# Optimization experiments

Hardware: AMD Instinct MI355X
Metric: run time of the kernel (lower is better)

## Reference

```python
import jax, jax.numpy as jnp
import numpy as np

B, N, M, T, D, NH = 64, 1024, 32, 8, 512, 8
OUT = 1000
NSO, NSA = N // 4, N // 8
DH = D // NH


def _conv(x, w, b):
    y = jax.lax.conv_general_dilated(x, w, (1, 1), 'SAME', dimension_numbers=('NCHW', 'OIHW', 'NCHW'))
    return y + b[None, :, None, None]


def _bn(x, g, b):
    # BatchNorm2d in train mode: per-batch statistics over (B, H, W)
    m = x.mean(axis=(0, 2, 3), keepdims=True)
    v = x.var(axis=(0, 2, 3), keepdims=True)
    return (x - m) * jax.lax.rsqrt(v + 1e-5) * g[None, :, None, None] + b[None, :, None, None]


def _mp2(x):
    b_, c, h, w = x.shape
    return x.reshape(b_, c, h // 2, 2, w // 2, 2).max(axis=(3, 5))


def _ln(x, g, b):
    m = x.mean(-1, keepdims=True)
    v = x.var(-1, keepdims=True)
    return (x - m) * jax.lax.rsqrt(v + 1e-5) * g + b


def _glu(x):
    a, b = jnp.split(x, 2, axis=-1)
    return a * jax.nn.sigmoid(b)


def setup_inputs():
    ks = iter(jax.random.split(jax.random.key(0), 64))

    def nrm(shape, fan_in):
        return jax.random.normal(next(ks), shape, jnp.float32) / np.float32(np.sqrt(fan_in))

    inp = {}
    inp['x'] = jax.random.normal(next(ks), (B, 3, 64, 64), jnp.float32)
    inp['c1w'] = nrm((16, 3, 3, 3), 27); inp['c1b'] = jnp.zeros((16,))
    inp['bn1g'] = jnp.ones((16,)); inp['bn1b'] = jnp.zeros((16,))
    inp['c2w'] = nrm((32, 16, 3, 3), 144); inp['c2b'] = jnp.zeros((32,))
    inp['bn2g'] = jnp.ones((32,)); inp['bn2b'] = jnp.zeros((32,))
    inp['c3w'] = nrm((64, 32, 3, 3), 288); inp['c3b'] = jnp.zeros((64,))
    inp['bn3g'] = jnp.ones((64,)); inp['bn3b'] = jnp.zeros((64,))
    inp['c4w'] = nrm((64, 64, 3, 3), 576); inp['c4b'] = jnp.zeros((64,))
    inp['bn4g'] = jnp.ones((64,)); inp['bn4b'] = jnp.zeros((64,))
    inp['fc1w'] = nrm((256, 256), 256); inp['fc1b'] = jnp.zeros((256,))
    inp['fc2w'] = nrm((128, D), 128); inp['fc2b'] = jnp.zeros((D,))
    inp['kvw'] = nrm((D, D), D); inp['kvb'] = jnp.zeros((D,))
    inp['kvlg'] = jnp.ones((D,)); inp['kvlb'] = jnp.zeros((D,))
    inp['synw'] = nrm((D + N, 2 * N), D + N); inp['synb'] = jnp.zeros((2 * N,))
    inp['synlg'] = jnp.ones((N,)); inp['synlb'] = jnp.zeros((N,))
    inp['nlm_w1'] = nrm((N, M, 256), M); inp['nlm_b1'] = jnp.zeros((N, 256))
    inp['nlm_w2'] = nrm((N, 128), 128); inp['nlm_b2'] = jnp.zeros((N,))
    inp['start_act'] = nrm((N,), N)
    inp['start_trace'] = nrm((N, M), N + M)
    inp['dec_a'] = jax.random.uniform(next(ks), (NSA,), jnp.float32, 0.0, 3.0)
    inp['dec_o'] = jax.random.uniform(next(ks), (NSO,), jnp.float32, 0.0, 3.0)
    inp['qw'] = nrm((NSA, D), NSA); inp['qb'] = jnp.zeros((D,))
    inp['attn_inw'] = nrm((D, 3 * D), D); inp['attn_inb'] = jnp.zeros((3 * D,))
    inp['attn_ow'] = nrm((D, D), D); inp['attn_ob'] = jnp.zeros((D,))
    inp['op_w1'] = nrm((NSO, 256), NSO); inp['op_b1'] = jnp.zeros((256,))
    inp['op_l1g'] = jnp.ones((256,)); inp['op_l1b'] = jnp.zeros((256,))
    inp['op_w2'] = nrm((256, 64), 256); inp['op_b2'] = jnp.zeros((64,))
    inp['op_l2g'] = jnp.ones((64,)); inp['op_l2b'] = jnp.zeros((64,))
    inp['op_w3'] = nrm((64, OUT), 64); inp['op_b3'] = jnp.zeros((OUT,))
    inp['aL'] = jax.random.randint(next(ks), (NSA,), 0, N)
    inp['aR'] = jax.random.randint(next(ks), (NSA,), 0, N)
    inp['oL'] = jax.random.randint(next(ks), (NSO,), 0, N)
    inp['oR'] = jax.random.randint(next(ks), (NSO,), 0, N)
    inp['task_idx'] = 0
    return inp


def _forward(x, c1w, c1b, bn1g, bn1b, c2w, c2b, bn2g, bn2b, c3w, c3b, bn3g, bn3b, c4w, c4b, bn4g, bn4b, fc1w, fc1b, fc2w, fc2b, kvw, kvb, kvlg, kvlb, synw, synb, synlg, synlb, nlm_w1, nlm_b1, nlm_w2, nlm_b2, start_act, start_trace, dec_a, dec_o, qw, qb, attn_inw, attn_inb, attn_ow, attn_ob, op_w1, op_b1, op_l1g, op_l1b, op_w2, op_b2, op_l2g, op_l2b, op_w3, op_b3, aL, aR, oL, oR):
    # --- AdaptiveCNNEncoder (3-channel branch) ---
    h = jax.nn.relu(_bn(_conv(x, c1w, c1b), bn1g, bn1b))
    h = jax.nn.relu(_bn(_conv(h, c2w, c2b), bn2g, bn2b))
    h = _mp2(h)
    h = jax.nn.relu(_bn(_conv(h, c3w, c3b), bn3g, bn3b))
    h = _mp2(h)
    h = jax.nn.relu(_bn(_conv(h, c4w, c4b), bn4g, bn4b))
    b_, c, hh, ww = h.shape
    # AdaptiveAvgPool2d((2,2)): mean over equal blocks (16x16 -> 2x2)
    h = h.reshape(b_, c, 2, hh // 2, 2, ww // 2).mean(axis=(3, 5)).reshape(b_, c * 4)
    enc = _glu(h @ fc1w + fc1b) @ fc2w + fc2b            # (B, D)
    kv = _ln(enc @ kvw + kvb, kvlg, kvlb)                # single kv token

    Wq, Wk, Wv = jnp.split(attn_inw, 3, axis=1)
    bq, bk, bv = jnp.split(attn_inb, 3)
    kh = (kv @ Wk + bk).reshape(B, NH, DH)
    vh = (kv @ Wv + bv).reshape(B, NH, DH)

    r_a = jnp.exp(-jnp.clip(dec_a, 0.0, 15.0))           # (NSA,)
    r_o = jnp.exp(-jnp.clip(dec_o, 0.0, 15.0))           # (NSO,)

    act0 = jnp.broadcast_to(start_act, (B, N))
    trace0 = jnp.broadcast_to(start_trace, (B, N, M))
    ao0 = act0[:, oL] * act0[:, oR]                      # initial out-sync accumulators
    bo0 = jnp.ones_like(ao0)
    inv_log_out = np.float32(1.0 / np.log(OUT))
    inv_sqrt_dh = np.float32(1.0 / np.sqrt(DH))

    def tick(carry, t):
        act, trace, aa, ba, ao, bo = carry
        pp = act[:, aL] * act[:, aR]
        first = (t == 0)
        aa = jnp.where(first, pp, r_a * aa + pp)
        ba = jnp.where(first, jnp.ones_like(ba), r_a * ba + 1.0)
        sync_a = aa * jax.lax.rsqrt(ba + 1e-8)
        qv = sync_a @ qw + qb
        qh = (qv @ Wq + bq).reshape(B, NH, DH)
        logits = jnp.einsum('bhd,bhd->bh', qh, kh) * inv_sqrt_dh
        w = jax.nn.softmax(logits[..., None], axis=-1)[..., 0]  # single key -> ones
        attn_out = (w[..., None] * vh).reshape(B, D) @ attn_ow + attn_ob
        pre = jnp.concatenate([attn_out, act], axis=-1)
        state = _ln(_glu(pre @ synw + synb), synlg, synlb)
        trace = jnp.concatenate([trace[:, :, 1:], state[:, :, None]], axis=-1)
        # per-neuron private MLPs, batched: (B,N,M)x(N,M,256) -> GLU -> (N,128) -> scalar
        hid = _glu(jnp.einsum('bnm,nmh->bnh', trace, nlm_w1) + nlm_b1)
        act = jnp.einsum('bnh,nh->bn', hid, nlm_w2) + nlm_b2
        po = act[:, oL] * act[:, oR]
        ao = r_o * ao + po
        bo = r_o * bo + 1.0
        sync_o = ao * jax.lax.rsqrt(bo + 1e-8)
        h1 = jax.nn.relu(_ln(sync_o @ op_w1 + op_b1, op_l1g, op_l1b))
        h2 = jax.nn.relu(_ln(h1 @ op_w2 + op_b2, op_l2g, op_l2b))
        pred = h2 @ op_w3 + op_b3
        p = jax.nn.softmax(pred, axis=-1)
        ent = -jnp.sum(p * jnp.log(p + 1e-10), axis=-1)
        ne = ent * inv_log_out
        cert = jnp.stack([ne, 1.0 - ne], axis=-1)
        return (act, trace, aa, ba, ao, bo), (pred, cert)

    carry0 = (act0, trace0, jnp.zeros((B, NSA), jnp.float32), jnp.zeros((B, NSA), jnp.float32), ao0, bo0)
    _, (preds, certs) = jax.lax.scan(tick, carry0, jnp.arange(T))
    return jnp.transpose(preds, (1, 2, 0)), jnp.transpose(certs, (1, 2, 0))


def reference(x, c1w, c1b, bn1g, bn1b, c2w, c2b, bn2g, bn2b, c3w, c3b, bn3g, bn3b, c4w, c4b, bn4g, bn4b, fc1w, fc1b, fc2w, fc2b, kvw, kvb, kvlg, kvlb, synw, synb, synlg, synlb, nlm_w1, nlm_b1, nlm_w2, nlm_b2, start_act, start_trace, dec_a, dec_o, qw, qb, attn_inw, attn_inb, attn_ow, attn_ob, op_w1, op_b1, op_l1g, op_l1b, op_w2, op_b2, op_l2g, op_l2b, op_w3, op_b3, aL, aR, oL, oR, task_idx):
    del task_idx  # single task; all task-indexed params are for task 0
    return _forward(x, c1w, c1b, bn1g, bn1b, c2w, c2b, bn2g, bn2b, c3w, c3b, bn3g, bn3b, c4w, c4b, bn4g, bn4b, fc1w, fc1b, fc2w, fc2b, kvw, kvb, kvlg, kvlb, synw, synb, synlg, synlb, nlm_w1, nlm_b1, nlm_w2, nlm_b2, start_act, start_trace, dec_a, dec_o, qw, qb, attn_inw, attn_inb, attn_ow, attn_ob, op_w1, op_b1, op_l1g, op_l1b, op_w2, op_b2, op_l2g, op_l2b, op_w3, op_b3, aL, aR, oL, oR)
```

## Files before the change

kernel.cpp:

```cpp
#include <hip/hip_runtime.h>
#include <math.h>

constexpr int B_ = 64, N_ = 1024, M_ = 32, T_ = 8;
constexpr int OUT_ = 1000, NSO_ = 256;

#define DEVFN __device__ __forceinline__

typedef __attribute__((ext_vector_type(8))) short bf16x8;
typedef __attribute__((ext_vector_type(4))) float f32x4;

DEVFN float blockReduceSum(float v, float* buf) {
  int t = threadIdx.x;
  buf[t] = v; __syncthreads();
  for (int off = blockDim.x >> 1; off > 0; off >>= 1) {
    if (t < off) buf[t] += buf[t + off];
    __syncthreads();
  }
  float r = buf[0];
  __syncthreads();
  return r;
}

DEVFN float sigmoidf_(float x) { return 1.f / (1.f + __expf(-x)); }

// ... 13 lines not shown
  __syncthreads();
  if (w == 0) {
    float x = (ln < NW) ? red[ln] : 0.f;
    #pragma unroll
    for (int o = 8; o > 0; o >>= 1) x += __shfl_xor(x, o);
    if (ln == 0) red[0] = x;
  }
  __syncthreads();
  float r = red[0];
  __syncthreads();
  return r;
}

template<int NW>
DEVFN float bmax(float v, float* red) {
  #pragma unroll
  for (int o = 32; o > 0; o >>= 1) v = fmaxf(v, __shfl_xor(v, o));
  int w = threadIdx.x >> 6, ln = threadIdx.x & 63;
  if (ln == 0) red[w] = v;
  __syncthreads();
  if (w == 0) {
    float x = (ln < NW) ? red[ln] : -INFINITY;
    #pragma unroll
    for (int o = 8; o > 0; o >>= 1) x = fmaxf(x, __shfl_xor(x, o));
    if (ln == 0) red[0] = x;
  }
  __syncthreads();
  float r = red[0];
  __syncthreads();
  return r;
}

__global__ __launch_bounds__(256)
void k_w1t(const float* __restrict__ w1, unsigned short* __restrict__ w1t) {
  int n = blockIdx.x;
  __shared__ float tile[32][260];
  const float* src = w1 + (size_t)n * 8192;
  for (int i = threadIdx.x; i < 8192; i += 256)
    tile[i >> 8][i & 255] = src[i];
  __syncthreads();
  int c = threadIdx.x;
  unsigned short* dst = w1t + ((size_t)n * 256 + c) * 32;
  #pragma unroll
  for (int q = 0; q < 8; ++q) {
    ushort4 o;
    o.x = f2bf(tile[q * 4 + 0][c]); o.y = f2bf(tile[q * 4 + 1][c]);
    o.z = f2bf(tile[q * 4 + 2][c]); o.w = f2bf(tile[q * 4 + 3][c]);
    *reinterpret_cast<ushort4*>(dst + q * 4) = o;
  }
}

__global__ __launch_bounds__(256)
void k_synwt(const float* __restrict__ synw2, unsigned short* __restrict__ Bt) {
  int j0 = blockIdx.x * 64, k0 = blockIdx.y * 64;
  __shared__ float tile[64][65];
  for (int i = threadIdx.x; i < 4096; i += 256) {
    int kk = i >> 6, jj = i & 63;
    tile[kk][jj] = synw2[(size_t)(k0 + kk) * 2048 + j0 + jj];
  }
  __syncthreads();
  int jj = threadIdx.x >> 2, kq = (threadIdx.x & 3) * 16;
  unsigned short* dst = Bt + (size_t)(j0 + jj) * 1024 + k0 + kq;
  #pragma unroll
  for (int q = 0; q < 4; ++q) {
    ushort4 o;
    o.x = f2bf(tile[kq + q * 4 + 0][jj]); o.y = f2bf(tile[kq + q * 4 + 1][jj]);
    o.z = f2bf(tile[kq + q * 4 + 2][jj]); o.w = f2bf(tile[kq + q * 4 + 3][jj]);
    *reinterpret_cast<ushort4*>(dst + q * 4) = o;
  }
}

template<int CIN, int COUT, int HW, int TY, int XV, int CICH, int MODE, int KSPLIT, int COSPLIT>
__global__ __launch_bounds__(256)
void k_conv_tiled(const float* __restrict__ in, const float* __restrict__ wgl,
                  const float2* __restrict__ ssin, float* __restrict__ outp) {
  constexpr int XQ = HW / XV;
  constexpr int NCG = 4;
  constexpr int CPT = COUT / (NCG * COSPLIT);
  constexpr int PADW = HW + 8;
  constexpr int NROW = TY + 2;
  constexpr int CINB = CIN / KSPLIT;
  constexpr int NCH = CINB / CICH;
  static_assert(XQ * TY == 64, "spatial threads per co-group must be 64");
  __shared__ __align__(16) float ins[CICH][NROW][PADW];

  const int b   = blockIdx.x;
  const int y0  = blockIdx.y * TY;
  const int cs  = (COSPLIT > 1) ? (int)(blockIdx.z % COSPLIT) : 0;
  const int ks  = (KSPLIT > 1) ? (int)(blockIdx.z / COSPLIT) : 0;
  const int co0 = cs * (COUT / COSPLIT);
  const int tid = threadIdx.x;
  const int sp  = tid & 63;
  const int cg  = __builtin_amdgcn_readfirstlane(tid >> 6);
  const int xq  = sp % XQ;
  const int yr  = sp / XQ;
  const int x0  = xq * XV;

  float acc[CPT][XV];
  #pragma unroll
  for (int j = 0; j < CPT; ++j)
    #pragma unroll
    for (int k = 0; k < XV; ++k) acc[j][k] = 0.f;

  for (int ch = 0; ch < NCH; ++ch) {
    const int ci0 = ks * CINB + ch * CICH;
    __syncthreads();
    constexpr int NEL = CICH * NROW * PADW;
    for (int i = tid; i < NEL; i += 256) {
      int col = i % PADW;
      int row = (i / PADW) % NROW;
      int ci  = i / (PADW * NROW);
      int gx = col - 4;
      int gy = y0 + row - 1;
      float v = 0.f;
      if (gx >= 0 && gx < HW && gy >= 0 && gy < HW) {
        if (MODE == 0) {
          v = in[((size_t)(b * CIN + ci0 + ci) * HW + gy) * HW + gx];
        } else if (MODE == 1) {
          float2 s = ssin[ci0 + ci];
          v = fmaxf(fmaf(in[((size_t)(b * CIN + ci0 + ci) * HW + gy) * HW + gx], s.x, s.y), 0.f);
        } else {
          float2 s = ssin[ci0 + ci];
          const float* p = in + ((size_t)(b * CIN + ci0 + ci) * (2 * HW) + 2 * gy) * (2 * HW) + 2 * gx;
          float v0 = fmaf(p[0],          s.x, s.y);
          float v1 = fmaf(p[1],          s.x, s.y);
          float v2 = fmaf(p[2 * HW],     s.x, s.y);
          float v3 = fmaf(p[2 * HW + 1], s.x, s.y);
          v = fmaxf(fmaxf(fmaxf(v0, v1), fmaxf(v2, v3)), 0.f);
        }
      }
      ins[ci][row][col] = v;
    }
    __syncthreads();

    for (int ci = 0; ci < CICH; ++ci) {
      const float* wci = wgl + ((size_t)(co0 + cg * CPT) * CIN + (ci0 + ci)) * 9;
      #pragma unroll
      for (int dy = 0; dy < 3; ++dy) {
        const float* r = &ins[ci][yr + dy][x0 + 4];
        float win[XV + 2];
        win[0] = r[-1];
        if constexpr (XV == 4) {
          float4 m = *reinterpret_cast<const float4*>(r);
          win[1] = m.x; win[2] = m.y; win[3] = m.z; win[4] = m.w;
        } else if constexpr (XV == 2) {
          float2 m = *reinterpret_cast<const float2*>(r);
          win[1] = m.x; win[2] = m.y;
        } else {
          win[1] = r[0];
        }
        win[XV + 1] = r[XV];
        #pragma unroll
        for (int j = 0; j < CPT; ++j) {
          const float* wj = wci + (size_t)j * CIN * 9 + dy * 3;
          float w0 = wj[0], w1 = wj[1], w2 = wj[2];
          #pragma unroll
          for (int k = 0; k < XV; ++k)
            acc[j][k] = fmaf(win[k], w0, fmaf(win[k + 1], w1, fmaf(win[k + 2], w2, acc[j][k])));
        }
      }
    }
  }

  const size_t pofs = (size_t)ks * B_ * COUT * HW * HW;
  #pragma unroll
  for (int j = 0; j < CPT; ++j) {
    float* op = outp + pofs + (((size_t)b * COUT + co0 + cg * CPT + j) * HW + y0 + yr) * HW + x0;
    if constexpr (XV == 4)
      *reinterpret_cast<float4*>(op) = make_float4(acc[j][0], acc[j][1], acc[j][2], acc[j][3]);
    else if constexpr (XV == 2)
      *reinterpret_cast<float2*>(op) = make_float2(acc[j][0], acc[j][1]);
    else
      *op = acc[j][0];
  }
}

template<int C, int HW2, int NS>
__global__ __launch_bounds__(256)
void k_bn_stats(const float* __restrict__ x, float* __restrict__ part) {
  int c = blockIdx.x, s = blockIdx.y, ns = gridDim.y;
  const int Npc = B_ * HW2;
  constexpr size_t PSTR = (size_t)B_ * C * HW2;
  float s1 = 0.f, s2 = 0.f;
  for (int ii = s * 256 + threadIdx.x; ii < Npc; ii += ns * 256) {
    int b = ii / HW2, pos = ii % HW2;
    size_t base = ((size_t)b * C + c) * HW2 + pos;
    float v = x[base];
    #pragma unroll
    for (int q = 1; q < NS; ++q) v += x[base + q * PSTR];
    s1 += v; s2 += v * v;
  }
  __shared__ float r1[256], r2[256];
  r1[threadIdx.x] = s1; r2[threadIdx.x] = s2; __syncthreads();
  for (int off = 128; off > 0; off >>= 1) {
    if (threadIdx.x < off) { r1[threadIdx.x] += r1[threadIdx.x + off]; r2[threadIdx.x] += r2[threadIdx.x + off]; }
    __syncthreads();
  }
  if (threadIdx.x == 0) {
    part[(c * ns + s) * 2 + 0] = r1[0];
    part[(c * ns + s) * 2 + 1] = r2[0];
  }
}

__global__ void k_bn_finalize(const float* __restrict__ part, int C, int ns, float inv_n,
                              const float* __restrict__ g, const float* __restrict__ bb,
                              float2* __restrict__ ss) {
  int c = threadIdx.x;
  if (c >= C) return;
  float s1 = 0.f, s2 = 0.f;
  for (int s = 0; s < ns; ++s) { s1 += part[(c * ns + s) * 2]; s2 += part[(c * ns + s) * 2 + 1]; }
  float m = s1 * inv_n;
  float var = s2 * inv_n - m * m;
  float rstd = rsqrtf(var + 1e-5f);
  float sc = g[c] * rstd;
  ss[c] = make_float2(sc, bb[c] - m * sc);
}

__global__ __launch_bounds__(256)
void k_avgpool_bn(const float* __restrict__ x, const float2* __restrict__ ss,
                  float* __restrict__ outp) {
  constexpr size_t PSTR = (size_t)B_ * 64 * 256;
  int idx = blockIdx.x * 256 + threadIdx.x;
  if (idx >= B_ * 256) return;
  int b = idx >> 8;
  int r = idx & 255;
  int c = r >> 2, i = (r >> 1) & 1, j = r & 1;
  float2 s = ss[c];
  const float* p = x + ((size_t)(b * 64 + c) * 16 + i * 8) * 16 + j * 8;
  float sum = 0.f;
  #pragma unroll
  for (int yy = 0; yy < 8; ++yy)
    #pragma unroll
    for (int xx = 0; xx < 8; ++xx) {
      size_t o = yy * 16 + xx;
      float v = p[o] + p[o + PSTR] + p[o + 2 * PSTR] + p[o + 3 * PSTR];
      sum += fmaxf(fmaf(v, s.x, s.y), 0.f);
    }
  outp[idx] = sum * (1.f / 64.f);
}

template<int K, int NOUT>
__global__ __launch_bounds__(256)
void k_gemm_part(const float* __restrict__ A, const float* __restrict__ W, int ldw,
                 float* __restrict__ part) {
  int jt = blockIdx.x, ks = blockIdx.y;
  int k0 = ks * 64;
  __shared__ float As[64][65];
  for (int i = threadIdx.x; i < 4096; i += 256) {
    int r = i >> 6, c = i & 63;
    As[r][c] = A[(size_t)r * K + k0 + c];
  }
  __syncthreads();
  int jsub = threadIdx.x & 31;
  int bg = threadIdx.x >> 5;
  int j = jt * 32 + jsub;
  float acc[8] = {0.f, 0.f, 0.f, 0.f, 0.f, 0.f, 0.f, 0.f};
  const float* wp = W + (size_t)k0 * ldw + j;
  #pragma unroll 8
  for (int kk = 0; kk < 64; ++kk) {
    float w = wp[(size_t)kk * ldw];
    #pragma unroll
    for (int r = 0; r < 8; ++r) acc[r] = fmaf(As[bg * 8 + r][kk], w, acc[r]);
  }
  float* pp = part + (size_t)ks * 64 * NOUT + j;
  #pragma unroll
  for (int r = 0; r < 8; ++r) pp[(size_t)(bg * 8 + r) * NOUT] = acc[r];
}

__global__ __launch_bounds__(256)
void k_syn_mfma(const unsigned short* __restrict__ Abf, const unsigned short* __restrict__ Bt,
                float* __restrict__ part) {
  const int jt = blockIdx.x, ks = blockIdx.y;
  const int w = threadIdx.x >> 6, lane = threadIdx.x & 63;
  const int col = lane & 15, kg = lane >> 4;
  const int jbase = jt * 128 + w * 32;
  const int k0 = ks * 128;
  f32x4 acc[4][2];
  #pragma unroll
  for (int mt = 0; mt < 4; ++mt)
    #pragma unroll
    for (int nt = 0; nt < 2; ++nt) acc[mt][nt] = (f32x4){0.f, 0.f, 0.f, 0.f};

  #pragma unroll
  for (int kb = 0; kb < 4; ++kb) {
    const int kk = k0 + kb * 32 + kg * 8;
    bf16x8 a[4], bfr[2];
    #pragma unroll
    for (int mt = 0; mt < 4; ++mt)
      a[mt] = *reinterpret_cast<const bf16x8*>(Abf + (size_t)(mt * 16 + col) * 1024 + kk);
    #pragma unroll
    for (int nt = 0; nt < 2; ++nt)
      bfr[nt] = *reinterpret_cast<const bf16x8*>(Bt + (size_t)(jbase + nt * 16 + col) * 1024 + kk);
    #pragma unroll
    for (int mt = 0; mt < 4; ++mt)
      #pragma unroll
      for (int nt = 0; nt < 2; ++nt)
        acc[mt][nt] = __builtin_amdgcn_mfma_f32_16x16x32_bf16(a[mt], bfr[nt], acc[mt][nt], 0, 0, 0);
  }
  #pragma unroll
  for (int mt = 0; mt < 4; ++mt)
    #pragma unroll
    for (int nt = 0; nt < 2; ++nt) {
      int j = jbase + nt * 16 + col;
      int b0 = mt * 16 + kg * 4;
      #pragma unroll
      for (int r = 0; r < 4; ++r)
        part[((size_t)ks * 64 + b0 + r) * 2048 + j] = acc[mt][nt][r];
    }
}

template<int NOUT, int NO_FIN, int KS, bool GLU_, bool LN_>
__global__ __launch_bounds__(256)
void k_fc_reduce(const float* __restrict__ part, const float* __restrict__ bias, int bstride,
                 const float* __restrict__ lng, const float* __restrict__ lnb,
                 float* __restrict__ outp) {
// ... 63 lines not shown

__global__ __launch_bounds__(256)
void k_init(const float* __restrict__ sa, const float* __restrict__ st,
            const int* __restrict__ oL, const int* __restrict__ oR,
            float* __restrict__ act, unsigned short* __restrict__ act_bf,
            unsigned short* __restrict__ trace,
            float* __restrict__ ao, float* __restrict__ bo) {
  int idx = blockIdx.x * 256 + threadIdx.x;
  if (idx < B_ * N_ * M_) {
    int n = idx >> 11, m = idx & 31;
    trace[idx] = f2bf(st[n * 32 + m]);
  }
  if (idx < B_ * N_) {
    float v = sa[idx % N_];
    act[idx] = v;
    act_bf[idx] = f2bf(v);
  }
  if (idx < B_ * NSO_) {
    int i = idx % NSO_;
    ao[idx] = sa[oL[i]] * sa[oR[i]];
    bo[idx] = 1.f;
  }
}

__global__ __launch_bounds__(128)
void k_nlm_mfma(const unsigned short* __restrict__ trace, const unsigned short* __restrict__ w1t,
                const float* __restrict__ b1, const float* __restrict__ w2,
                const float* __restrict__ b2, float* __restrict__ act,
                unsigned short* __restrict__ act_bf, int tick) {
  const int w = threadIdx.x >> 6, lane = threadIdx.x & 63;
  const int n = blockIdx.x * 2 + w;
  const int col = lane & 15, kg = lane >> 4;
  __shared__ __align__(16) unsigned short ldsA[2][64][40];

  {
    const uint4* src = reinterpret_cast<const uint4*>(trace + ((size_t)n * 64 + lane) * 32);
    uint4 r0 = src[0], r1 = src[1], r2 = src[2], r3 = src[3];
    uint4* d = reinterpret_cast<uint4*>(&ldsA[w][lane][0]);
    d[0] = r0; d[1] = r1; d[2] = r2; d[3] = r3;
  }

  bf16x8 bf[16];
  float b1v[16], w2v[8];
  #pragma unroll
  for (int nt = 0; nt < 16; ++nt) {
    bf[nt] = *reinterpret_cast<const bf16x8*>(w1t + (((size_t)n * 256 + nt * 16 + col) * 32 + kg * 8));
    b1v[nt] = b1[n * 256 + nt * 16 + col];
  }
  #pragma unroll
  for (int nt = 0; nt < 8; ++nt) w2v[nt] = w2[n * 128 + nt * 16 + col];
  const float b2n = b2[n];
  const int kbase = kg * 8 + ((tick + 1) & 31);
  __syncthreads();

  #pragma unroll
  for (int mt = 0; mt < 4; ++mt) {
    const int brow = mt * 16 + col;
    bf16x8 af;
    #pragma unroll
    for (int j = 0; j < 8; ++j)
      af[j] = (short)ldsA[w][brow][(kbase + j) & 31];
    f32x4 acc[16];
    #pragma unroll
    for (int nt = 0; nt < 16; ++nt)
      acc[nt] = __builtin_amdgcn_mfma_f32_16x16x32_bf16(af, bf[nt], (f32x4){0.f, 0.f, 0.f, 0.f}, 0, 0, 0);
    float v0 = 0.f, v1 = 0.f, v2 = 0.f, v3 = 0.f;
    #pragma unroll
    for (int nt = 0; nt < 8; ++nt) {
      f32x4 za = acc[nt], zb = acc[nt + 8];
      float ba = b1v[nt], bg = b1v[nt + 8], wv = w2v[nt];
      v0 = fmaf((za[0] + ba) * sigmoidf_(zb[0] + bg), wv, v0);
      v1 = fmaf((za[1] + ba) * sigmoidf_(zb[1] + bg), wv, v1);
      v2 = fmaf((za[2] + ba) * sigmoidf_(zb[2] + bg), wv, v2);
      v3 = fmaf((za[3] + ba) * sigmoidf_(zb[3] + bg), wv, v3);
    }
    #pragma unroll
    for (int o = 1; o <= 8; o <<= 1) {
      v0 += __shfl_xor(v0, o); v1 += __shfl_xor(v1, o);
      v2 += __shfl_xor(v2, o); v3 += __shfl_xor(v3, o);
    }
    if (col == 0) {
      int b0 = mt * 16 + kg * 4;
      float r0 = v0 + b2n, r1 = v1 + b2n, r2 = v2 + b2n, r3 = v3 + b2n;
      act[(size_t)(b0 + 0) * 1024 + n] = r0;
      act[(size_t)(b0 + 1) * 1024 + n] = r1;
      act[(size_t)(b0 + 2) * 1024 + n] = r2;
      act[(size_t)(b0 + 3) * 1024 + n] = r3;
      act_bf[(size_t)(b0 + 0) * 1024 + n] = f2bf(r0);
      act_bf[(size_t)(b0 + 1) * 1024 + n] = f2bf(r1);
      act_bf[(size_t)(b0 + 2) * 1024 + n] = f2bf(r2);
      act_bf[(size_t)(b0 + 3) * 1024 + n] = f2bf(r3);
    }
  }
}

__global__ __launch_bounds__(1024)
void k_outpath(const float* __restrict__ act, float* __restrict__ ao, float* __restrict__ bo,
               const float* __restrict__ dec_o, const int* __restrict__ oL, const int* __restrict__ oR,
               const float* __restrict__ opw1, const float* __restrict__ opb1,
               const float* __restrict__ l1g, const float* __restrict__ l1b,
               const float* __restrict__ opw2, const float* __restrict__ opb2,
               const float* __restrict__ l2g, const float* __restrict__ l2b,
               const float* __restrict__ opw3, const float* __restrict__ opb3,
               float* __restrict__ outp, int tick) {
  int b = blockIdx.x, t = threadIdx.x;
  __shared__ float red[16];
  __shared__ float syo[256], h1s[256], h2s[64];
  __shared__ float zp1[4][256];
  __shared__ float zp2[16][64];
  const float* actb = act + (size_t)b * 1024;

  if (t < 256) {
    float po = actb[oL[t]] * actb[oR[t]];
    float r = __expf(-fminf(fmaxf(dec_o[t], 0.f), 15.f));
    int ai = b * 256 + t;
    float av = fmaf(r, ao[ai], po);
    float bv = fmaf(r, bo[ai], 1.f);
    ao[ai] = av; bo[ai] = bv;
    syo[t] = av * rsqrtf(bv + 1e-8f);
  }
  __syncthreads();

  {
    int j = t & 255, ks = t >> 8;
    float z = 0.f;
    const float* wcol = opw1 + j;
    #pragma unroll 8
    for (int k = ks * 64; k < ks * 64 + 64; ++k) z = fmaf(syo[k], wcol[k * 256], z);
    zp1[ks][j] = z;
  }
  __syncthreads();
  float h1v = 0.f;
  if (t < 256) h1v = zp1[0][t] + zp1[1][t] + zp1[2][t] + zp1[3][t] + opb1[t];
  float s1 = bsum<16>(t < 256 ? h1v : 0.f, red);
  float s2 = bsum<16>(t < 256 ? h1v * h1v : 0.f, red);
  if (t < 256) {
    float mu = s1 * (1.f / 256.f);
    float rstd = rsqrtf(s2 * (1.f / 256.f) - mu * mu + 1e-5f);
    h1s[t] = fmaxf(fmaf((h1v - mu) * rstd, l1g[t], l1b[t]), 0.f);
  }
  __syncthreads();

  {
    int j = t & 63, ks = t >> 6;
    float z = 0.f;
    const float* wcol = opw2 + j;
    #pragma unroll
    for (int k = ks * 16; k < ks * 16 + 16; ++k) z = fmaf(h1s[k], wcol[k * 64], z);
    zp2[ks][j] = z;
  }
  __syncthreads();
  if (t < 64) {
    float z2 = opb2[t];
    #pragma unroll
    for (int ks = 0; ks < 16; ++ks) z2 += zp2[ks][t];
    float a1 = z2, a2 = z2 * z2;
    #pragma unroll
    for (int o = 32; o > 0; o >>= 1) { a1 += __shfl_xor(a1, o); a2 += __shfl_xor(a2, o); }
    float mu2 = a1 * (1.f / 64.f);
    float rs2 = rsqrtf(a2 * (1.f / 64.f) - mu2 * mu2 + 1e-5f);
    h2s[t] = fmaxf(fmaf((z2 - mu2) * rs2, l2g[t], l2b[t]), 0.f);
  }
  __syncthreads();

  float z3 = 0.f;
  if (t < OUT_) {
    z3 = opb3[t];
    const float* wcol = opw3 + t;
    #pragma unroll 8
    for (int k = 0; k < 64; ++k) z3 = fmaf(h2s[k], wcol[k * OUT_], z3);
    outp[(size_t)b * (OUT_ * T_) + (size_t)t * T_ + tick] = z3;
  }
  float mx = bmax<16>(t < OUT_ ? z3 : -INFINITY, red);
  float e = (t < OUT_) ? __expf(z3 - mx) : 0.f;
  float S = bsum<16>(e, red);
  float inv = 1.f / S;
  float ep = 0.f;
  if (t < OUT_) {
    float p = e * inv;
    ep = p * __logf(p + 1e-10f);
  }
  float ent = -bsum<16>(ep, red);
  if (t == 0) {
    float ne = ent * (1.f / logf(1000.f));
    outp[(size_t)B_ * OUT_ * T_ + (size_t)b * 2 * T_ + tick]      = ne;
    outp[(size_t)B_ * OUT_ * T_ + (size_t)b * 2 * T_ + T_ + tick] = 1.f - ne;
  }
}

extern "C" void kernel_launch(void* const* d_in, const int* in_sizes, int n_in,
                              void* d_out, int out_size, void* d_ws, size_t ws_size,
                              hipStream_t stream) {
  (void)in_sizes; (void)n_in; (void)out_size; (void)ws_size;
  const float* x      = (const float*)d_in[0];
  const float* c1w    = (const float*)d_in[1];
  const float* bn1g   = (const float*)d_in[3];
  const float* bn1b   = (const float*)d_in[4];
// ... 14 lines not shown
  const float* kvb    = (const float*)d_in[22];
  const float* kvlg   = (const float*)d_in[23];
  const float* kvlb   = (const float*)d_in[24];
  const float* synw   = (const float*)d_in[25];
  const float* synb   = (const float*)d_in[26];
  const float* synlg  = (const float*)d_in[27];
  const float* synlb  = (const float*)d_in[28];
  const float* nlmw1  = (const float*)d_in[29];
  const float* nlmb1  = (const float*)d_in[30];
  const float* nlmw2  = (const float*)d_in[31];
  const float* nlmb2  = (const float*)d_in[32];
  const float* sact   = (const float*)d_in[33];
  const float* strc   = (const float*)d_in[34];
  const float* dec_o  = (const float*)d_in[36];
  const float* attn_inw = (const float*)d_in[39];
  const float* attn_inb = (const float*)d_in[40];
  const float* attn_ow  = (const float*)d_in[41];
  const float* attn_ob  = (const float*)d_in[42];
  const float* opw1   = (const float*)d_in[43];
  const float* opb1   = (const float*)d_in[44];
  const float* opl1g  = (const float*)d_in[45];
  const float* opl1b  = (const float*)d_in[46];
  const float* opw2   = (const float*)d_in[47];
  const float* opb2   = (const float*)d_in[48];
  const float* opl2g  = (const float*)d_in[49];
  const float* opl2b  = (const float*)d_in[50];
  const float* opw3   = (const float*)d_in[51];
  const float* opb3   = (const float*)d_in[52];
  const int*   oL     = (const int*)d_in[55];
  const int*   oR     = (const int*)d_in[56];
  float* outp = (float*)d_out;
  float* ws   = (float*)d_ws;

  float* c2raw = ws;
  float* c4part= ws;
  float* c1raw = ws + 8388608;
  float* c3raw = ws + 8388608;
  float* part  = ws + 4194304;
  unsigned short* trace_bf = (unsigned short*)(ws + 6291456);
  float* act   = ws + 8388608;
  float* syncst= ws + 8454144;
  float* pooled= ws + 8585216;
  float* ench  = ws + 8601600;
  float* enc   = ws + 8609792;
  float* kvbuf = ws + 8642560;
  float* vhbuf = ws + 8675328;
  float* aout  = ws + 8708096;
  float* ao    = ws + 8740864;
  float* bo    = ws + 8757248;
  unsigned short* w1t_bf   = (unsigned short*)(ws + 8777728);
  unsigned short* synw2t_bf= (unsigned short*)(ws + 12972032);
  float* bnpart= ws + 14020608;
  float2* bnss = (float2*)(ws + 14024704);
  unsigned short* act_bf = (unsigned short*)(ws + 14028800);

  k_conv_tiled<3,16,64,4,4,3,0,1,1><<<dim3(64,16),256,0,stream>>>(x, c1w, nullptr, c1raw);
  k_bn_stats<16,4096,1><<<dim3(16,32),256,0,stream>>>(c1raw, bnpart);
  k_bn_finalize<<<1,64,0,stream>>>(bnpart, 16, 32, 1.f/(float)(B_*4096), bn1g, bn1b, bnss);

  k_conv_tiled<16,32,64,2,2,16,1,1,1><<<dim3(64,32),256,0,stream>>>(c1raw, c2w, bnss, c2raw);
  k_bn_stats<32,4096,1><<<dim3(32,32),256,0,stream>>>(c2raw, bnpart);
  k_bn_finalize<<<1,64,0,stream>>>(bnpart, 32, 32, 1.f/(float)(B_*4096), bn2g, bn2b, bnss);

  k_conv_tiled<32,64,32,4,2,16,2,1,2><<<dim3(64,8,2),256,0,stream>>>(c2raw, c3w, bnss, c3raw);
  k_bn_stats<64,1024,1><<<dim3(64,16),256,0,stream>>>(c3raw, bnpart);
  k_bn_finalize<<<1,64,0,stream>>>(bnpart, 64, 16, 1.f/(float)(B_*1024), bn3g, bn3b, bnss);

  k_conv_tiled<64,64,16,4,1,16,2,4,1><<<dim3(64,4,4),256,0,stream>>>(c3raw, c4w, bnss, c4part);

  k_w1t<<<1024,256,0,stream>>>(nlmw1, w1t_bf);
  k_synwt<<<dim3(32,16),256,0,stream>>>(synw + (size_t)512 * 2048, synw2t_bf);

  k_bn_stats<64,256,4><<<dim3(64,8),256,0,stream>>>(c4part, bnpart);
  k_bn_finalize<<<1,64,0,stream>>>(bnpart, 64, 8, 1.f/(float)(B_*256), bn4g, bn4b, bnss);
  k_avgpool_bn<<<64,256,0,stream>>>(c4part, bnss, pooled);

  k_gemm_part<256,256><<<dim3(8,4),256,0,stream>>>(pooled, fc1w, 256, part);
  k_fc_reduce<256,128,4,true,false><<<64,256,0,stream>>>(part, fc1b, 0, nullptr, nullptr, ench);
  k_gemm_part<128,512><<<dim3(16,2),256,0,stream>>>(ench, fc2w, 512, part);
  k_fc_reduce<512,512,2,false,false><<<64,256,0,stream>>>(part, fc2b, 0, nullptr, nullptr, enc);
  k_gemm_part<512,512><<<dim3(16,8),256,0,stream>>>(enc, kvw, 512, part);
  k_fc_reduce<512,512,8,false,true><<<64,256,0,stream>>>(part, kvb, 0, kvlg, kvlb, kvbuf);
  k_gemm_part<512,512><<<dim3(16,8),256,0,stream>>>(kvbuf, attn_inw + 1024, 1536, part);
  k_fc_reduce<512,512,8,false,false><<<64,256,0,stream>>>(part, attn_inb + 1024, 0, nullptr, nullptr, vhbuf);
  k_gemm_part<512,512><<<dim3(16,8),256,0,stream>>>(vhbuf, attn_ow, 512, part);
  k_fc_reduce<512,512,8,false,false><<<64,256,0,stream>>>(part, attn_ob, 0, nullptr, nullptr, aout);
  k_gemm_part<512,2048><<<dim3(64,8),256,0,stream>>>(aout, synw, 2048, part);
  k_fc_reduce<2048,2048,8,false,false><<<64,256,0,stream>>>(part, synb, 0, nullptr, nullptr, syncst);

  k_init<<<8192,256,0,stream>>>(sact, strc, oL, oR, act, act_bf, trace_bf, ao, bo);

  for (int t = 0; t < T_; ++t) {
    k_syn_mfma<<<dim3(16,8),256,0,stream>>>(act_bf, synw2t_bf, part);
    k_syn_reduce<<<64,1024,0,stream>>>(part, syncst, synlg, synlb, trace_bf, t);
    k_nlm_mfma<<<512,128,0,stream>>>(trace_bf, w1t_bf, nlmb1, nlmw2, nlmb2, act, act_bf, t);
    k_outpath<<<64,1024,0,stream>>>(act, ao, bo, dec_o, oL, oR,
                                    opw1, opb1, opl1g, opl1b,
                                    opw2, opb2, opl2g, opl2b,
                                    opw3, opb3, outp, t);
  }
}
```

Before: 596.5 us.

## Move conv2-4 to bf16 MFMA implicit GEMM with NHWC padded inputs

Conv layers 2-4 move from FP32 scalar direct convolution to bf16 MFMA implicit-GEMM kernels. Separate prep kernels apply BN+ReLU (and maxpool) and write zero-padded NHWC bf16 inputs, and weights are pre-transposed to bf16 per tap. BN statistics and avgpool are rewritten for NHWC layout, and the split-K partial sums for conv4 are dropped. This cuts the FP32 FMA cost of the conv stack but adds extra prep passes and global traffic, and lowers precision to bf16.

After: 642.0 us, median of 2. 1.08x slower.

```diff
diff --git a/kernel.cpp b/kernel.cpp
--- a/kernel.cpp
+++ b/kernel.cpp
@@ -69,6 +69,25 @@
 }
 
 __global__ __launch_bounds__(256)
+void k_wprep(const float* __restrict__ c2w, const float* __restrict__ c3w,
+             const float* __restrict__ c4w, unsigned short* __restrict__ wt2,
+             unsigned short* __restrict__ wt3, unsigned short* __restrict__ wt4) {
+  int i = blockIdx.x * 256 + threadIdx.x;
+  if (i < 5120) {
+    int tap = i / 512, co = (i / 16) % 32, ci = i & 15;
+    wt2[i] = (tap < 9) ? f2bf(c2w[(co * 16 + ci) * 9 + tap]) : 0;
+  } else if (i < 5120 + 18432) {
+    int j = i - 5120;
+    int tap = j / 2048, co = (j / 32) % 64, ci = j & 31;
+    wt3[j] = f2bf(c3w[(co * 32 + ci) * 9 + tap]);
+  } else if (i < 5120 + 18432 + 36864) {
+    int j = i - 5120 - 18432;
+    int tap = j / 4096, co = (j / 64) % 64, ci = j & 63;
+    wt4[j] = f2bf(c4w[(co * 64 + ci) * 9 + tap]);
+  }
+}
+
+__global__ __launch_bounds__(256)
 void k_w1t(const float* __restrict__ w1, unsigned short* __restrict__ w1t) {
   int n = blockIdx.x;
   __shared__ float tile[32][260];
@@ -107,85 +126,48 @@
   }
 }
 
-template<int CIN, int COUT, int HW, int TY, int XV, int CICH, int MODE, int KSPLIT, int COSPLIT>
+template<int CIN, int COUT, int HW, int TY, int XV, int CICH>
 __global__ __launch_bounds__(256)
 void k_conv_tiled(const float* __restrict__ in, const float* __restrict__ wgl,
-                  const float2* __restrict__ ssin, float* __restrict__ outp) {
+                  float* __restrict__ outp) {
   constexpr int XQ = HW / XV;
-  constexpr int NCG = 4;
-  constexpr int CPT = COUT / (NCG * COSPLIT);
+  constexpr int CPT = COUT / 4;
   constexpr int PADW = HW + 8;
   constexpr int NROW = TY + 2;
-  constexpr int CINB = CIN / KSPLIT;
-  constexpr int NCH = CINB / CICH;
-  static_assert(XQ * TY == 64, "spatial threads per co-group must be 64");
+  constexpr int NCH = CIN / CICH;
+  static_assert(XQ * TY == 64, "");
   __shared__ __align__(16) float ins[CICH][NROW][PADW];
-
-  const int b   = blockIdx.x;
-  const int y0  = blockIdx.y * TY;
-  const int cs  = (COSPLIT > 1) ? (int)(blockIdx.z % COSPLIT) : 0;
-  const int ks  = (KSPLIT > 1) ? (int)(blockIdx.z / COSPLIT) : 0;
-  const int co0 = cs * (COUT / COSPLIT);
-  const int tid = threadIdx.x;
-  const int sp  = tid & 63;
-  const int cg  = __builtin_amdgcn_readfirstlane(tid >> 6);
-  const int xq  = sp % XQ;
-  const int yr  = sp / XQ;
-  const int x0  = xq * XV;
-
+  const int b = blockIdx.x, y0 = blockIdx.y * TY, tid = threadIdx.x;
+  const int sp = tid & 63;
+  const int cg = __builtin_amdgcn_readfirstlane(tid >> 6);
+  const int xq = sp % XQ, yr = sp / XQ, x0 = xq * XV;
   float acc[CPT][XV];
   #pragma unroll
   for (int j = 0; j < CPT; ++j)
     #pragma unroll
     for (int k = 0; k < XV; ++k) acc[j][k] = 0.f;
-
   for (int ch = 0; ch < NCH; ++ch) {
-    const int ci0 = ks * CINB + ch * CICH;
+    const int ci0 = ch * CICH;
     __syncthreads();
     constexpr int NEL = CICH * NROW * PADW;
     for (int i = tid; i < NEL; i += 256) {
-      int col = i % PADW;
-      int row = (i / PADW) % NROW;
-      int ci  = i / (PADW * NROW);
-      int gx = col - 4;
-      int gy = y0 + row - 1;
+      int col = i % PADW, row = (i / PADW) % NROW, ci = i / (PADW * NROW);
+      int gx = col - 4, gy = y0 + row - 1;
       float v = 0.f;
-      if (gx >= 0 && gx < HW && gy >= 0 && gy < HW) {
-        if (MODE == 0) {
-          v = in[((size_t)(b * CIN + ci0 + ci) * HW + gy) * HW + gx];
-        } else if (MODE == 1) {
-          float2 s = ssin[ci0 + ci];
-          v = fmaxf(fmaf(in[((size_t)(b * CIN + ci0 + ci) * HW + gy) * HW + gx], s.x, s.y), 0.f);
-        } else {
-          float2 s = ssin[ci0 + ci];
-          const float* p = in + ((size_t)(b * CIN + ci0 + ci) * (2 * HW) + 2 * gy) * (2 * HW) + 2 * gx;
-          float v0 = fmaf(p[0],          s.x, s.y);
-          float v1 = fmaf(p[1],          s.x, s.y);
-          float v2 = fmaf(p[2 * HW],     s.x, s.y);
-          float v3 = fmaf(p[2 * HW + 1], s.x, s.y);
-          v = fmaxf(fmaxf(fmaxf(v0, v1), fmaxf(v2, v3)), 0.f);
-        }
-      }
+      if (gx >= 0 && gx < HW && gy >= 0 && gy < HW)
+        v = in[((size_t)(b * CIN + ci0 + ci) * HW + gy) * HW + gx];
       ins[ci][row][col] = v;
     }
     __syncthreads();
-
     for (int ci = 0; ci < CICH; ++ci) {
-      const float* wci = wgl + ((size_t)(co0 + cg * CPT) * CIN + (ci0 + ci)) * 9;
+      const float* wci = wgl + ((size_t)(cg * CPT) * CIN + (ci0 + ci)) * 9;
       #pragma unroll
       for (int dy = 0; dy < 3; ++dy) {
         const float* r = &ins[ci][yr + dy][x0 + 4];
         float win[XV + 2];
         win[0] = r[-1];
-        if constexpr (XV == 4) {
-          float4 m = *reinterpret_cast<const float4*>(r);
-          win[1] = m.x; win[2] = m.y; win[3] = m.z; win[4] = m.w;
-        } else if constexpr (XV == 2) {
-          float2 m = *reinterpret_cast<const float2*>(r);
-          win[1] = m.x; win[2] = m.y;
-        } else {
-          win[1] = r[0];
-        }
+        float4 m = *reinterpret_cast<const float4*>(r);
+        win[1] = m.x; win[2] = m.y; win[3] = m.z; win[4] = m.w;
         win[XV + 1] = r[XV];
         #pragma unroll
         for (int j = 0; j < CPT; ++j) {
@@ -198,33 +180,22 @@
       }
     }
   }
-
-  const size_t pofs = (size_t)ks * B_ * COUT * HW * HW;
   #pragma unroll
   for (int j = 0; j < CPT; ++j) {
-    float* op = outp + pofs + (((size_t)b * COUT + co0 + cg * CPT + j) * HW + y0 + yr) * HW + x0;
-    if constexpr (XV == 4)
-      *reinterpret_cast<float4*>(op) = make_float4(acc[j][0], acc[j][1], acc[j][2], acc[j][3]);
-    else if constexpr (XV == 2)
-      *reinterpret_cast<float2*>(op) = make_float2(acc[j][0], acc[j][1]);
-    else
-      *op = acc[j][0];
-  }
-}
-
-template<int C, int HW2, int NS>
+    float* op = outp + (((size_t)b * COUT + cg * CPT + j) * HW + y0 + yr) * HW + x0;
+    *reinterpret_cast<float4*>(op) = make_float4(acc[j][0], acc[j][1], acc[j][2], acc[j][3]);
+  }
+}
+
+template<int C, int HW2>
 __global__ __launch_bounds__(256)
 void k_bn_stats(const float* __restrict__ x, float* __restrict__ part) {
   int c = blockIdx.x, s = blockIdx.y, ns = gridDim.y;
   const int Npc = B_ * HW2;
-  constexpr size_t PSTR = (size_t)B_ * C * HW2;
   float s1 = 0.f, s2 = 0.f;
   for (int ii = s * 256 + threadIdx.x; ii < Npc; ii += ns * 256) {
     int b = ii / HW2, pos = ii % HW2;
-    size_t base = ((size_t)b * C + c) * HW2 + pos;
-    float v = x[base];
-    #pragma unroll
-    for (int q = 1; q < NS; ++q) v += x[base + q * PSTR];
+    float v = x[((size_t)b * C + c) * HW2 + pos];
     s1 += v; s2 += v * v;
   }
   __shared__ float r1[256], r2[256];
@@ -236,6 +207,29 @@
   if (threadIdx.x == 0) {
     part[(c * ns + s) * 2 + 0] = r1[0];
     part[(c * ns + s) * 2 + 1] = r2[0];
+  }
+}
+
+template<int C, int NPX>
+__global__ __launch_bounds__(256)
+void k_bn_stats_nhwc(const float* __restrict__ x, float* __restrict__ part) {
+  constexpr int G = 256 / C;
+  int s = blockIdx.x, ns = gridDim.x;
+  int c = threadIdx.x % C, g = threadIdx.x / C;
+  float s1 = 0.f, s2 = 0.f;
+  for (int p = s * G + g; p < NPX; p += ns * G) {
+    float v = x[(size_t)p * C + c];
+    s1 += v; s2 += v * v;
+  }
+  __shared__ float r1[256], r2[256];
+  r1[threadIdx.x] = s1; r2[threadIdx.x] = s2; __syncthreads();
+  for (int off = 128; off >= C; off >>= 1) {
+    if (threadIdx.x < off) { r1[threadIdx.x] += r1[threadIdx.x + off]; r2[threadIdx.x] += r2[threadIdx.x + off]; }
+    __syncthreads();
+  }
+  if (threadIdx.x < C) {
+    part[(c * ns + s) * 2 + 0] = r1[c];
+    part[(c * ns + s) * 2 + 1] = r2[c];
   }
 }
 
@@ -254,26 +248,174 @@
 }
 
 __global__ __launch_bounds__(256)
+void k_prep2(const float* __restrict__ c1raw, const float2* __restrict__ ss,
+             unsigned short* __restrict__ inp2) {
+  int b = blockIdx.x, yp = blockIdx.y;
+  unsigned short* orow = inp2 + ((size_t)(b * 66 + yp) * 66) * 16;
+  if (yp == 0 || yp == 65) {
+    for (int i = threadIdx.x; i < 66 * 16; i += 256) orow[i] = 0;
+    return;
+  }
+  int y = yp - 1;
+  __shared__ float lds[16][65];
+  for (int i = threadIdx.x; i < 1024; i += 256) {
+    int ci = i >> 6, x = i & 63;
+    float2 s = ss[ci];
+    lds[ci][x] = fmaxf(fmaf(c1raw[((size_t)(b * 16 + ci) * 64 + y) * 64 + x], s.x, s.y), 0.f);
+  }
+  __syncthreads();
+  for (int i = threadIdx.x; i < 66 * 16; i += 256) {
+    int xp = i >> 4, ci = i & 15;
+    orow[i] = (xp == 0 || xp == 65) ? 0 : f2bf(lds[ci][xp - 1]);
+  }
+}
+
+__global__ __launch_bounds__(256)
+void k_conv2_mfma(const unsigned short* __restrict__ inp2, const unsigned short* __restrict__ wt2,
+                  float* __restrict__ c2out) {
+  const int b = blockIdx.x, y = blockIdx.y;
+  const int w = threadIdx.x >> 6, lane = threadIdx.x & 63;
+  const int col = lane & 15, kg = lane >> 4;
+  const int p0 = w * 16;
+  f32x4 acc0 = {0.f, 0.f, 0.f, 0.f}, acc1 = {0.f, 0.f, 0.f, 0.f};
+  #pragma unroll
+  for (int pair = 0; pair < 5; ++pair) {
+    int tap = pair * 2 + (kg >> 1);
+    int dy = (tap < 9) ? tap / 3 : 2;
+    int dx = (tap < 9) ? tap % 3 : 2;
+    bf16x8 af = *reinterpret_cast<const bf16x8*>(
+        inp2 + ((size_t)(b * 66 + y + dy) * 66 + (p0 + col + dx)) * 16 + (kg & 1) * 8);
+    bf16x8 b0 = *reinterpret_cast<const bf16x8*>(wt2 + ((size_t)tap * 32 + col) * 16 + (kg & 1) * 8);
+    bf16x8 b1 = *reinterpret_cast<const bf16x8*>(wt2 + ((size_t)tap * 32 + 16 + col) * 16 + (kg & 1) * 8);
+    acc0 = __builtin_amdgcn_mfma_f32_16x16x32_bf16(af, b0, acc0, 0, 0, 0);
+    acc1 = __builtin_amdgcn_mfma_f32_16x16x32_bf16(af, b1, acc1, 0, 0, 0);
+  }
+  float* orow = c2out + ((size_t)(b * 64 + y) * 64) * 32;
+  #pragma unroll
+  for (int r = 0; r < 4; ++r) {
+    int x = p0 + kg * 4 + r;
+    orow[x * 32 + col]      = acc0[r];
+    orow[x * 32 + 16 + col] = acc1[r];
+  }
+}
+
+__global__ __launch_bounds__(256)
+void k_prep3(const float* __restrict__ c2out, const float2* __restrict__ ss,
+             unsigned short* __restrict__ inp3) {
+  int b = blockIdx.x, yp = blockIdx.y;
+  unsigned short* orow = inp3 + ((size_t)(b * 34 + yp) * 34) * 32;
+  if (yp == 0 || yp == 33) {
+    for (int i = threadIdx.x; i < 34 * 32; i += 256) orow[i] = 0;
+    return;
+  }
+  int y = yp - 1;
+  for (int i = threadIdx.x; i < 34 * 32; i += 256) {
+    int xp = i >> 5, ci = i & 31;
+    if (xp == 0 || xp == 33) { orow[i] = 0; continue; }
+    int x = xp - 1;
+    float2 s = ss[ci];
+    const float* p = c2out + ((size_t)(b * 64 + 2 * y) * 64 + 2 * x) * 32 + ci;
+    float v0 = fmaf(p[0],         s.x, s.y);
+    float v1 = fmaf(p[32],        s.x, s.y);
+    float v2 = fmaf(p[64 * 32],   s.x, s.y);
+    float v3 = fmaf(p[64 * 32 + 32], s.x, s.y);
+    orow[i] = f2bf(fmaxf(fmaxf(fmaxf(v0, v1), fmaxf(v2, v3)), 0.f));
+  }
+}
+
+__global__ __launch_bounds__(256)
+void k_conv3_mfma(const unsigned short* __restrict__ inp3, const unsigned short* __restrict__ wt3,
+                  float* __restrict__ c3out) {
+  const int b = blockIdx.x, y = blockIdx.y;
+  const int w = threadIdx.x >> 6, lane = threadIdx.x & 63;
+  const int col = lane & 15, kg = lane >> 4;
+  const int p0 = (w & 1) * 16, cb = (w >> 1) * 32;
+  f32x4 acc0 = {0.f, 0.f, 0.f, 0.f}, acc1 = {0.f, 0.f, 0.f, 0.f};
+  #pragma unroll
+  for (int tap = 0; tap < 9; ++tap) {
+    int dy = tap / 3, dx = tap % 3;
+    bf16x8 af = *reinterpret_cast<const bf16x8*>(
+        inp3 + ((size_t)(b * 34 + y + dy) * 34 + (p0 + col + dx)) * 32 + kg * 8);
+    bf16x8 b0 = *reinterpret_cast<const bf16x8*>(wt3 + ((size_t)tap * 64 + cb + col) * 32 + kg * 8);
+    bf16x8 b1 = *reinterpret_cast<const bf16x8*>(wt3 + ((size_t)tap * 64 + cb + 16 + col) * 32 + kg * 8);
+    acc0 = __builtin_amdgcn_mfma_f32_16x16x32_bf16(af, b0, acc0, 0, 0, 0);
+    acc1 = __builtin_amdgcn_mfma_f32_16x16x32_bf16(af, b1, acc1, 0, 0, 0);
+  }
+  float* orow = c3out + ((size_t)(b * 32 + y) * 32) * 64;
+  #pragma unroll
+  for (int r = 0; r < 4; ++r) {
+    int x = p0 + kg * 4 + r;
+    orow[x * 64 + cb + col]      = acc0[r];
+    orow[x * 64 + cb + 16 + col] = acc1[r];
+  }
+}
+
+__global__ __launch_bounds__(256)
+void k_prep4(const float* __restrict__ c3out, const float2* __restrict__ ss,
+             unsigned short* __restrict__ inp4) {
+  int b = blockIdx.x, yp = blockIdx.y;
+  unsigned short* orow = inp4 + ((size_t)(b * 18 + yp) * 18) * 64;
+  if (yp == 0 || yp == 17) {
+    for (int i = threadIdx.x; i < 18 * 64; i += 256) orow[i] = 0;
+    return;
+  }
+  int y = yp - 1;
+  for (int i = threadIdx.x; i < 18 * 64; i += 256) {
+    int xp = i >> 6, ci = i & 63;
+    if (xp == 0 || xp == 17) { orow[i] = 0; continue; }
+    int x = xp - 1;
+    float2 s = ss[ci];
+    const float* p = c3out + ((size_t)(b * 32 + 2 * y) * 32 + 2 * x) * 64 + ci;
+    float v0 = fmaf(p[0],          s.x, s.y);
+    float v1 = fmaf(p[64],         s.x, s.y);
+    float v2 = fmaf(p[32 * 64],    s.x, s.y);
+    float v3 = fmaf(p[32 * 64 + 64], s.x, s.y);
+    orow[i] = f2bf(fmaxf(fmaxf(fmaxf(v0, v1), fmaxf(v2, v3)), 0.f));
+  }
+}
+
+__global__ __launch_bounds__(256)
+void k_conv4_mfma(const unsigned short* __restrict__ inp4, const unsigned short* __restrict__ wt4,
+                  float* __restrict__ c4out) {
+  const int b = blockIdx.x, y = blockIdx.y;
+  const int w = threadIdx.x >> 6, lane = threadIdx.x & 63;
+  const int col = lane & 15, kg = lane >> 4;
+  const int cb = w * 16;
+  f32x4 acc = {0.f, 0.f, 0.f, 0.f};
+  #pragma unroll
+  for (int tap = 0; tap < 9; ++tap) {
+    int dy = tap / 3, dx = tap % 3;
+    #pragma unroll
+    for (int kc = 0; kc < 2; ++kc) {
+      bf16x8 af = *reinterpret_cast<const bf16x8*>(
+          inp4 + ((size_t)(b * 18 + y + dy) * 18 + (col + dx)) * 64 + kc * 32 + kg * 8);
+      bf16x8 bfr = *reinterpret_cast<const bf16x8*>(
+          wt4 + ((size_t)tap * 64 + cb + col) * 64 + kc * 32 + kg * 8);
+      acc = __builtin_amdgcn_mfma_f32_16x16x32_bf16(af, bfr, acc, 0, 0, 0);
+    }
+  }
+  float* orow = c4out + ((size_t)(b * 16 + y) * 16) * 64;
+  #pragma unroll
+  for (int r = 0; r < 4; ++r)
+    orow[(kg * 4 + r) * 64 + cb + col] = acc[r];
+}
+
+__global__ __launch_bounds__(256)
 void k_avgpool_bn(const float* __restrict__ x, const float2* __restrict__ ss,
                   float* __restrict__ outp) {
-  constexpr size_t PSTR = (size_t)B_ * 64 * 256;
-  int idx = blockIdx.x * 256 + threadIdx.x;
-  if (idx >= B_ * 256) return;
-  int b = idx >> 8;
-  int r = idx & 255;
-  int c = r >> 2, i = (r >> 1) & 1, j = r & 1;
+  int b = blockIdx.x, t = threadIdx.x;
+  int c = t & 63, quad = t >> 6;
+  int i = quad >> 1, j = quad & 1;
   float2 s = ss[c];
-  const float* p = x + ((size_t)(b * 64 + c) * 16 + i * 8) * 16 + j * 8;
   float sum = 0.f;
   #pragma unroll
   for (int yy = 0; yy < 8; ++yy)
     #pragma unroll
     for (int xx = 0; xx < 8; ++xx) {
-      size_t o = yy * 16 + xx;
-      float v = p[o] + p[o + PSTR] + p[o + 2 * PSTR] + p[o + 3 * PSTR];
+      float v = x[((size_t)(b * 16 + i * 8 + yy) * 16 + j * 8 + xx) * 64 + c];
       sum += fmaxf(fmaf(v, s.x, s.y), 0.f);
     }
-  outp[idx] = sum * (1.f / 64.f);
+  outp[b * 256 + c * 4 + quad] = sum * (1.f / 64.f);
 }
 
 template<int K, int NOUT>
@@ -317,7 +459,6 @@
   for (int mt = 0; mt < 4; ++mt)
     #pragma unroll
     for (int nt = 0; nt < 2; ++nt) acc[mt][nt] = (f32x4){0.f, 0.f, 0.f, 0.f};
-
   #pragma unroll
   for (int kb = 0; kb < 4; ++kb) {
     const int kk = k0 + kb * 32 + kg * 8;
@@ -447,14 +588,12 @@
   const int n = blockIdx.x * 2 + w;
   const int col = lane & 15, kg = lane >> 4;
   __shared__ __align__(16) unsigned short ldsA[2][64][40];
-
   {
     const uint4* src = reinterpret_cast<const uint4*>(trace + ((size_t)n * 64 + lane) * 32);
     uint4 r0 = src[0], r1 = src[1], r2 = src[2], r3 = src[3];
     uint4* d = reinterpret_cast<uint4*>(&ldsA[w][lane][0]);
     d[0] = r0; d[1] = r1; d[2] = r2; d[3] = r3;
   }
-
   bf16x8 bf[16];
   float b1v[16], w2v[8];
   #pragma unroll
@@ -467,7 +606,6 @@
   const float b2n = b2[n];
   const int kbase = kg * 8 + ((tick + 1) & 31);
   __syncthreads();
-
   #pragma unroll
   for (int mt = 0; mt < 4; ++mt) {
     const int brow = mt * 16 + col;
@@ -524,7 +662,6 @@
   __shared__ float zp1[4][256];
   __shared__ float zp2[16][64];
   const float* actb = act + (size_t)b * 1024;
-
   if (t < 256) {
     float po = actb[oL[t]] * actb[oR[t]];
     float r = __expf(-fminf(fmaxf(dec_o[t], 0.f), 15.f));
@@ -535,7 +672,6 @@
     syo[t] = av * rsqrtf(bv + 1e-8f);
   }
   __syncthreads();
-
   {
     int j = t & 255, ks = t >> 8;
     float z = 0.f;
@@ -555,7 +691,6 @@
     h1s[t] = fmaxf(fmaf((h1v - mu) * rstd, l1g[t], l1b[t]), 0.f);
   }
   __syncthreads();
-
   {
     int j = t & 63, ks = t >> 6;
     float z = 0.f;
@@ -577,7 +712,6 @@
     h2s[t] = fmaxf(fmaf((z2 - mu2) * rs2, l2g[t], l2b[t]), 0.f);
   }
   __syncthreads();
-
   float z3 = 0.f;
   if (t < OUT_) {
     z3 = opb3[t];
@@ -658,10 +792,13 @@
   float* outp = (float*)d_out;
   float* ws   = (float*)d_ws;
 
-  float* c2raw = ws;
-  float* c4part= ws;
   float* c1raw = ws + 8388608;
-  float* c3raw = ws + 8388608;
+  unsigned short* inp2 = (unsigned short*)ws;
+  float* c2out = ws + 2230272;
+  unsigned short* inp3 = (unsigned short*)(ws + 10618880);
+  float* c3out = ws;
+  unsigned short* inp4 = (unsigned short*)(ws + 4194304);
+  float* c4out = ws + 4857856;
   float* part  = ws + 4194304;
   unsigned short* trace_bf = (unsigned short*)(ws + 6291456);
   float* act   = ws + 8388608;
@@ -676,30 +813,38 @@
   float* bo    = ws + 8757248;
   unsigned short* w1t_bf   = (unsigned short*)(ws + 8777728);
   unsigned short* synw2t_bf= (unsigned short*)(ws + 12972032);
-  float* bnpart= ws + 14020608;
-  float2* bnss = (float2*)(ws + 14024704);
   unsigned short* act_bf = (unsigned short*)(ws + 14028800);
-
-  k_conv_tiled<3,16,64,4,4,3,0,1,1><<<dim3(64,16),256,0,stream>>>(x, c1w, nullptr, c1raw);
-  k_bn_stats<16,4096,1><<<dim3(16,32),256,0,stream>>>(c1raw, bnpart);
+  unsigned short* wt2 = (unsigned short*)(ws + 14061568);
+  unsigned short* wt3 = (unsigned short*)(ws + 14064128);
+  unsigned short* wt4 = (unsigned short*)(ws + 14073344);
+  float* bnpart= ws + 14091776;
+  float2* bnss = (float2*)(ws + 14124544);
+
+  k_wprep<<<236,256,0,stream>>>(c2w, c3w, c4w, wt2, wt3, wt4);
+
+  k_conv_tiled<3,16,64,4,4,3><<<dim3(64,16),256,0,stream>>>(x, c1w, c1raw);
+  k_bn_stats<16,4096><<<dim3(16,32),256,0,stream>>>(c1raw, bnpart);
   k_bn_finalize<<<1,64,0,stream>>>(bnpart, 16, 32, 1.f/(float)(B_*4096), bn1g, bn1b, bnss);
 
-  k_conv_tiled<16,32,64,2,2,16,1,1,1><<<dim3(64,32),256,0,stream>>>(c1raw, c2w, bnss, c2raw);
-  k_bn_stats<32,4096,1><<<dim3(32,32),256,0,stream>>>(c2raw, bnpart);
-  k_bn_finalize<<<1,64,0,stream>>>(bnpart, 32, 32, 1.f/(float)(B_*4096), bn2g, bn2b, bnss);
-
-  k_conv_tiled<32,64,32,4,2,16,2,1,2><<<dim3(64,8,2),256,0,stream>>>(c2raw, c3w, bnss, c3raw);
-  k_bn_stats<64,1024,1><<<dim3(64,16),256,0,stream>>>(c3raw, bnpart);
-  k_bn_finalize<<<1,64,0,stream>>>(bnpart, 64, 16, 1.f/(float)(B_*1024), bn3g, bn3b, bnss);
-
-  k_conv_tiled<64,64,16,4,1,16,2,4,1><<<dim3(64,4,4),256,0,stream>>>(c3raw, c4w, bnss, c4part);
+  k_prep2<<<dim3(64,66),256,0,stream>>>(c1raw, bnss, inp2);
+  k_conv2_mfma<<<dim3(64,64),256,0,stream>>>(inp2, wt2, c2out);
+  k_bn_stats_nhwc<32,262144><<<256,256,0,stream>>>(c2out, bnpart);
+  k_bn_finalize<<<1,64,0,stream>>>(bnpart, 32, 256, 1.f/262144.f, bn2g, bn2b, bnss);
+
+  k_prep3<<<dim3(64,34),256,0,stream>>>(c2out, bnss, inp3);
+  k_conv3_mfma<<<dim3(64,32),256,0,stream>>>(inp3, wt3, c3out);
+  k_bn_stats_nhwc<64,65536><<<256,256,0,stream>>>(c3out, bnpart);
+  k_bn_finalize<<<1,64,0,stream>>>(bnpart, 64, 256, 1.f/65536.f, bn3g, bn3b, bnss);
+
+  k_prep4<<<dim3(64,18),256,0,stream>>>(c3out, bnss, inp4);
+  k_conv4_mfma<<<dim3(64,16),256,0,stream>>>(inp4, wt4, c4out);
 
   k_w1t<<<1024,256,0,stream>>>(nlmw1, w1t_bf);
   k_synwt<<<dim3(32,16),256,0,stream>>>(synw + (size_t)512 * 2048, synw2t_bf);
 
-  k_bn_stats<64,256,4><<<dim3(64,8),256,0,stream>>>(c4part, bnpart);
-  k_bn_finalize<<<1,64,0,stream>>>(bnpart, 64, 8, 1.f/(float)(B_*256), bn4g, bn4b, bnss);
-  k_avgpool_bn<<<64,256,0,stream>>>(c4part, bnss, pooled);
+  k_bn_stats_nhwc<64,16384><<<128,256,0,stream>>>(c4out, bnpart);
+  k_bn_finalize<<<1,64,0,stream>>>(bnpart, 64, 128, 1.f/16384.f, bn4g, bn4b, bnss);
+  k_avgpool_bn<<<64,256,0,stream>>>(c4out, bnss, pooled);
 
   k_gemm_part<256,256><<<dim3(8,4),256,0,stream>>>(pooled, fc1w, 256, part);
   k_fc_reduce<256,128,4,true,false><<<64,256,0,stream>>>(part, fc1b, 0, nullptr, nullptr, ench);
```
